# Kernel tuning notes

Hardware: AMD Instinct MI355X
Metric: run time of the kernel (lower is better)

Reference implementation:

```python
import jax, jax.numpy as jnp
import numpy as np

B, T, D_IN, D_OUT = 32, 1024, 512, 512


def _glorot(key, shape):
    fan_in, fan_out = shape[0], shape[1]
    limit = np.sqrt(6.0 / (fan_in + fan_out)).astype(np.float32)
    return jax.random.uniform(key, shape, jnp.float32, -limit, limit)


def setup_inputs() -> dict:
    key = jax.random.key(0)
    ks = jax.random.split(key, 10)
    inp = {
        "inputs": jax.random.normal(ks[0], (B, T, D_IN), jnp.float32),
        "init_states": jnp.zeros((2, B, D_OUT), jnp.float32),
        "Wi": _glorot(ks[1], (D_IN, D_OUT)), "Ui": _glorot(ks[2], (D_OUT, D_OUT)), "bi": jnp.ones((D_OUT,), jnp.float32),
        "Wf": _glorot(ks[3], (D_IN, D_OUT)), "Uf": _glorot(ks[4], (D_OUT, D_OUT)), "bf": jnp.ones((D_OUT,), jnp.float32),
        "Wc": _glorot(ks[5], (D_IN, D_OUT)), "Uc": _glorot(ks[6], (D_OUT, D_OUT)), "bc": jnp.ones((D_OUT,), jnp.float32),
        "Wo": _glorot(ks[7], (D_IN, D_OUT)), "Uo": _glorot(ks[8], (D_OUT, D_OUT)), "bo": jnp.ones((D_OUT,), jnp.float32),
    }
    return inp


def reference(inputs, init_states, Wi, Ui, bi, Wf, Uf, bf, Wc, Uc, bc, Wo, Uo, bo):
    # inputs: [B, T, D_in] (time_major=False), init_states: [2, B, H]
    x_t = jnp.transpose(inputs, (1, 0, 2))  # [T, B, D_in]
    h0, c0 = init_states[0], init_states[1]

    def step(carry, x):
        h, c = carry
        i = jax.nn.sigmoid(x @ Wi + h @ Ui + bi)
        f = jax.nn.sigmoid(x @ Wf + h @ Uf + bf)
        g = jnp.tanh(x @ Wc + h @ Uc + bc)
        c_new = f * c + i * g
        o = jax.nn.sigmoid(x @ Wo + h @ Uo + bo)
        h_new = o * jnp.tanh(c_new)
        return (h_new, c_new), h_new

    _, hs = jax.lax.scan(step, (h0, c0), x_t)  # hs: [T, B, H]
    # original: transpose scan output [T,2,B,H] -> [2,B,T,H] then take [0] (hidden stream)
    return jnp.transpose(hs, (1, 0, 2))  # [B, T, H]
```

## Files before the change

### kernel.cpp

```cpp
#include <hip/hip_runtime.h>


#define T_STEPS 1024
#define BATCH   32
#define DIN     512
#define H       512
#define NWG     64
#define HC      8
#define XSTRIDE 520
#define GSTRIDE 34
#define RECS_PER_PARITY 8192

typedef _Float16 half8  __attribute__((ext_vector_type(8)));
typedef _Float16 half4v __attribute__((ext_vector_type(4)));
typedef float    f32x4  __attribute__((ext_vector_type(4)));
typedef unsigned int u32;
typedef unsigned long long u64;
typedef u32 u32x4 __attribute__((ext_vector_type(4)));

#define AT_LD_U64(p)   __hip_atomic_load((const u64*)(p), __ATOMIC_RELAXED, __HIP_MEMORY_SCOPE_AGENT)
#define AT_ST_U64(p,v) __hip_atomic_store((u64*)(p), (v), __ATOMIC_RELAXED, __HIP_MEMORY_SCOPE_AGENT)

__device__ __forceinline__ float sigmoidf_(float x) {
    return 1.0f / (1.0f + __expf(-x));
}
__device__ __forceinline__ float tanhf_(float x) {
    return 1.0f - 2.0f / (1.0f + __expf(2.0f * x));
}

__global__ __launch_bounds__(512, 1) void lstm_pregate(
    const float* __restrict__ x,
    const float* __restrict__ Wi, const float* __restrict__ Wf,
    const float* __restrict__ Wc, const float* __restrict__ Wo,
    const float* __restrict__ bi, const float* __restrict__ bf,
    const float* __restrict__ bc, const float* __restrict__ bo,
    float* __restrict__ preg, int t0, int tc)
{
    __shared__ _Float16 xbuf[2 * BATCH * XSTRIDE];

    const int tid  = threadIdx.x;
    const int wg   = blockIdx.x;
    const int cb   = wg & 31;
    const int tq   = wg >> 5;
    const int tcq  = tc >> 3;
    const int tb   = t0 + tq * tcq;
    const int lane = tid & 63;
    const int wave = tid >> 6;
    const int mt   = wave & 1;
    const int gsel = wave >> 1;
    const int n_local = lane & 15;
    const int kq   = lane >> 4;
    const int row  = mt * 16 + n_local;
    const int hcol = cb * 16 + n_local;

    const float* Wmat = (gsel == 0) ? Wi : (gsel == 1) ? Wf : (gsel == 2) ? Wc : Wo;
    const float* bvec = (gsel == 0) ? bi : (gsel == 1) ? bf : (gsel == 2) ? bc : bo;
    const float bv = bvec[hcol];

    half8 bfrag[16];
    #pragma unroll
    for (int kk = 0; kk < 16; ++kk) {
        #pragma unroll
        for (int jj = 0; jj < 8; ++jj) {
            int k = kk * 32 + kq * 8 + jj;
            bfrag[kk][jj] = (_Float16)Wmat[k * H + hcol];
        }
    }

    auto stage = [&](int t, int buf) {
        const int sb = tid >> 4;
        const int so = (tid & 15) * 4;
        const float* xr = x + ((size_t)sb * T_STEPS + t) * DIN;
        _Float16* xb = &xbuf[buf * (BATCH * XSTRIDE)];
        #pragma unroll
        for (int q = 0; q < 8; ++q) {
            int colq = so + q * 64;
            float4 v = *(const float4*)(xr + colq);
            half4v hv = { (_Float16)v.x, (_Float16)v.y,
                          (_Float16)v.z, (_Float16)v.w };
            *(half4v*)&xb[sb * XSTRIDE + colq] = hv;
        }
    };

    stage(tb, 0);
    stage(tb + 1, 1);
    __syncthreads();

    for (int lt = 0; lt < tcq; ++lt) {
        f32x4 a0 = {0.f, 0.f, 0.f, 0.f};
        f32x4 a1 = {0.f, 0.f, 0.f, 0.f};
        const _Float16* xr2 =
            &xbuf[(lt & 1) * (BATCH * XSTRIDE) + row * XSTRIDE + kq * 8];
        #pragma unroll
        for (int kk = 0; kk < 16; kk += 2) {
            half8 v0 = *(const half8*)(xr2 + kk * 32);
            half8 v1 = *(const half8*)(xr2 + (kk + 1) * 32);
            a0 = __builtin_amdgcn_mfma_f32_16x16x32_f16(v0, bfrag[kk],     a0, 0, 0, 0);
            a1 = __builtin_amdgcn_mfma_f32_16x16x32_f16(v1, bfrag[kk + 1], a1, 0, 0, 0);
        }
        f32x4 aw;
        #pragma unroll
        for (int r = 0; r < 4; ++r) aw[r] = a0[r] + a1[r] + bv;

        const size_t base =
            (((size_t)(tb - t0 + lt) * 4 + gsel) * 512 + hcol) * 32
            + mt * 16 + kq * 4;
        *(f32x4*)&preg[base] = aw;

        __syncthreads();
        if (lt + 2 < tcq) stage(tb + lt + 2, lt & 1);
    }
}

__global__ __launch_bounds__(256, 1) void lstm_recur(
    const float* __restrict__ init_states,
    const float* __restrict__ Ui, const float* __restrict__ Uf,
    const float* __restrict__ Uc, const float* __restrict__ Uo,
    const float* __restrict__ preg,
    float* __restrict__ out,
    u64* __restrict__ hrec,
    float* __restrict__ cst,
    int t0, int tc)
{
    __shared__ u32 share[2][2][16][64][4];

    const int tid  = threadIdx.x;
    const int wg   = blockIdx.x;
    const int lane = tid & 63;
    const int wave = tid >> 6;
    const int mt   = wave & 1;
    const int nt   = wave >> 1;
    const int n_local = lane & 15;
    const int kq   = lane >> 4;
    const int row  = mt * 16 + n_local;

    const int gi   = n_local >> 2;
    const int cl   = n_local & 3;
    const int ejl  = nt * 4 + cl;
    const int wcol = wg * HC + ejl;
    const int eb   = mt * 16 + kq * 4 + gi;
    const int ecol = wcol;

    float c_state = (t0 == 0) ? init_states[BATCH * H + eb * H + ecol]
                              : cst[eb * H + ecol];

    const int widx = (wg >> 2) * 512 + (ejl >> 1) * 128 + eb * 4 + (wg & 3);

    if (t0 == 0) {
        _Float16 h0 = (_Float16)init_states[eb * H + ecol];
        u32 hu  = (u32)__builtin_bit_cast(unsigned short, h0);
        u32 oth = __shfl_down(hu, 1);
        if ((lane & 1) == 0)
            AT_ST_U64(&hrec[widx], ((u64)1u << 32) | (u64)(hu | (oth << 16)));
    }

    const float* Umat = (gi == 0) ? Ui : (gi == 1) ? Uf : (gi == 2) ? Uc : Uo;
    half8 bfrag[16];
    #pragma unroll
    for (int kk = 0; kk < 16; ++kk) {
        #pragma unroll
        for (int jj = 0; jj < 8; ++jj) {
            int k = kk * 32 + kq * 8 + jj;
            bfrag[kk][jj] = (_Float16)Umat[k * H + wcol];
        }
    }

    const size_t pgbase =
        ((size_t)gi * 512 + wcol) * 32 + mt * 16 + kq * 4;
    f32x4 pg = *(const f32x4*)&preg[pgbase];

    const int ridx_base = row * 4 + kq;
    const int kk0 = nt * 8;
    const bool q0 = (lane >> 2) & 1;
    const bool q1 = (lane >> 3) & 1;

    for (int lt = 0; lt < tc; ++lt) {
        const int gt = t0 + lt;
        const u64* rb = hrec + (size_t)(gt & 1) * RECS_PER_PARITY;
        const u32 target = (u32)(gt + 1);
        const int par = gt & 1;

        u64 rec[32];
        unsigned spins = 0;
        for (;;) {
            #pragma unroll
            for (int kk2 = 0; kk2 < 8; ++kk2) {
                #pragma unroll
                for (int s = 0; s < 4; ++s)
                    rec[kk2 * 4 + s] =
                        AT_LD_U64(&rb[(kk0 + kk2) * 512 + s * 128 + ridx_base]);
            }
            int ok = 1;
            #pragma unroll
            for (int i = 0; i < 32; ++i)
                ok &= ((u32)(rec[i] >> 32) == target);
            if (__all(ok)) break;
            if (++spins > 300000u) break;
        }

        #pragma unroll
        for (int kk2 = 0; kk2 < 8; ++kk2) {
            u32x4 v = { (u32)rec[kk2 * 4 + 0], (u32)rec[kk2 * 4 + 1],
                        (u32)rec[kk2 * 4 + 2], (u32)rec[kk2 * 4 + 3] };
            *(u32x4*)&share[par][mt][kk0 + kk2][lane][0] = v;
        }

        f32x4 pgn = pg;
        if (lt + 1 < tc)
            pgn = *(const f32x4*)&preg[(size_t)(lt + 1) * 65536 + pgbase];

        __syncthreads();

        u32x4 au[16];
        #pragma unroll
        for (int kk = 0; kk < 16; ++kk)
            au[kk] = *(const u32x4*)&share[par][mt][kk][lane][0];

        f32x4 acc  = pg;
        f32x4 acc2 = {0.f, 0.f, 0.f, 0.f};
        #pragma unroll
        for (int kk = 0; kk < 16; kk += 2) {
            union { u32x4 v; half8 h; } a0, a1;
            a0.v = au[kk];
            a1.v = au[kk + 1];
            acc  = __builtin_amdgcn_mfma_f32_16x16x32_f16(a0.h, bfrag[kk],     acc,  0, 0, 0);
            acc2 = __builtin_amdgcn_mfma_f32_16x16x32_f16(a1.h, bfrag[kk + 1], acc2, 0, 0, 0);
        }
        float a0v = acc[0] + acc2[0];
        float a1v = acc[1] + acc2[1];
        float a2v = acc[2] + acc2[2];
        float a3v = acc[3] + acc2[3];

        float t0_ = __shfl_xor(a1v, 4);
        float t1_ = __shfl_xor(a0v, 4);
        float t2_ = __shfl_xor(a3v, 4);
        float t3_ = __shfl_xor(a2v, 4);
        float b0 = q0 ? t0_ : a0v;
        float b1 = q0 ? a1v : t1_;
        float b2 = q0 ? t2_ : a2v;
        float b3 = q0 ? a3v : t3_;
        float u0 = __shfl_xor(b2, 8);
        float u1 = __shfl_xor(b3, 8);
        float u2 = __shfl_xor(b0, 8);
        float u3 = __shfl_xor(b1, 8);
        float pi  = q1 ? u0 : b0;
        float pf  = q1 ? u1 : b1;
        float pgg = q1 ? b2 : u2;
        float po  = q1 ? b3 : u3;

        float ig = sigmoidf_(pi);
        float fg = sigmoidf_(pf);
        float gg = tanhf_(pgg);
        float og = sigmoidf_(po);
        c_state  = fg * c_state + ig * gg;
        float h_val = og * tanhf_(c_state);

        if (gt + 1 < T_STEPS) {
            _Float16 hh = (_Float16)h_val;
            u32 hu  = (u32)__builtin_bit_cast(unsigned short, hh);
            u32 oth = __shfl_down(hu, 1);
            if ((lane & 1) == 0) {
                AT_ST_U64(&hrec[(size_t)((gt + 1) & 1) * RECS_PER_PARITY + widx],
                          ((u64)(u32)(gt + 2) << 32) | (u64)(hu | (oth << 16)));
            }
        }

        out[((size_t)eb * T_STEPS + gt) * H + ecol] = h_val;
        pg = pgn;
    }

    cst[eb * H + ecol] = c_state;
}

__global__ __launch_bounds__(256, 1) void lstm_persistent_fb(
    const float* __restrict__ x,
    const float* __restrict__ init_states,
    const float* __restrict__ Wi, const float* __restrict__ Ui, const float* __restrict__ bi,
    const float* __restrict__ Wf, const float* __restrict__ Uf, const float* __restrict__ bf,
    const float* __restrict__ Wc, const float* __restrict__ Uc, const float* __restrict__ bc,
    const float* __restrict__ Wo, const float* __restrict__ Uo, const float* __restrict__ bo,
    float* __restrict__ out,
    u64* __restrict__ hrec)
{
    __shared__ _Float16 xbuf[2 * BATCH * XSTRIDE];
    __shared__ float    gbuf[2 * BATCH * GSTRIDE];

    const int tid  = threadIdx.x;
    const int wg   = blockIdx.x;
    const int lane = tid & 63;
    const int wave = tid >> 6;
    const int mt   = wave & 1;
    const int nt   = wave >> 1;
    const int row  = mt * 16 + (lane & 15);
    const int kq   = lane >> 4;

    const int eb   = tid >> 3;
    const int ej   = tid & 7;
    const int ecol = wg * HC + ej;

    float c_state = init_states[BATCH * H + eb * H + ecol];
    {
        _Float16 h0 = (_Float16)init_states[eb * H + ecol];
        u32 hu  = (u32)__builtin_bit_cast(unsigned short, h0);
        u32 oth = __shfl_down(hu, 1);
        if ((tid & 1) == 0) {
            const int ridx = (wg >> 2) * 512 + (ej >> 1) * 128 + eb * 4 + (wg & 3);
            AT_ST_U64(&hrec[ridx], ((u64)1u << 32) | (u64)(hu | (oth << 16)));
        }
    }

    const int n_local = lane & 15;
    const int gi   = nt * 2 + (n_local >> 3);
    const int wcol = wg * HC + (n_local & 7);
    const float* Wmat = (gi == 0) ? Wi : (gi == 1) ? Wf : (gi == 2) ? Wc : Wo;
    const float* Umat = (gi == 0) ? Ui : (gi == 1) ? Uf : (gi == 2) ? Uc : Uo;

    half8 bfrag[32];
    #pragma unroll
    for (int kk = 0; kk < 16; ++kk) {
        #pragma unroll
        for (int jj = 0; jj < 8; ++jj) {
            int k = kk * 32 + kq * 8 + jj;
            bfrag[kk][jj]      = (_Float16)Wmat[k * H + wcol];
            bfrag[16 + kk][jj] = (_Float16)Umat[k * H + wcol];
        }
    }

    const float bi_v = bi[ecol], bf_v = bf[ecol], bc_v = bc[ecol], bo_v = bo[ecol];

    auto stage = [&](int t, int buf) {
        const int sb = tid >> 3;
        const int so = (tid & 7) * 4;
        const float* xr = x + ((size_t)sb * T_STEPS + t) * DIN;
        _Float16* xb = &xbuf[buf * (BATCH * XSTRIDE)];
        #pragma unroll
        for (int q = 0; q < 16; ++q) {
            int colq = so + q * 32;
            float4 v = *(const float4*)(xr + colq);
            half4v hv = { (_Float16)v.x, (_Float16)v.y,
                          (_Float16)v.z, (_Float16)v.w };
            *(half4v*)&xb[sb * XSTRIDE + colq] = hv;
        }
    };
    auto xmm = [&](int buf) -> f32x4 {
        f32x4 ax  = {0.f, 0.f, 0.f, 0.f};
        f32x4 ax2 = {0.f, 0.f, 0.f, 0.f};
        const _Float16* xr2 = &xbuf[buf * (BATCH * XSTRIDE) + row * XSTRIDE + kq * 8];
        #pragma unroll
        for (int kk = 0; kk < 16; kk += 2) {
            half8 a0 = *(const half8*)(xr2 + kk * 32);
            half8 a1 = *(const half8*)(xr2 + (kk + 1) * 32);
            ax  = __builtin_amdgcn_mfma_f32_16x16x32_f16(a0, bfrag[kk],     ax,  0, 0, 0);
            ax2 = __builtin_amdgcn_mfma_f32_16x16x32_f16(a1, bfrag[kk + 1], ax2, 0, 0, 0);
        }
        #pragma unroll
        for (int r = 0; r < 4; ++r) ax[r] += ax2[r];
        return ax;
    };

    stage(0, 0);
    stage(1, 1);
    __syncthreads();
    f32x4 acc_x = xmm(0);

    const int ridx_base = row * 4 + kq;
    const int widx = (wg >> 2) * 512 + (ej >> 1) * 128 + eb * 4 + (wg & 3);

    for (int t = 0; t < T_STEPS; ++t) {
        const u64* rb = hrec + (size_t)(t & 1) * RECS_PER_PARITY;
        const u32 target = (u32)(t + 1);

        u64 rec[64];
        unsigned spins = 0;
        for (;;) {
            #pragma unroll
            for (int kk = 0; kk < 16; ++kk) {
                #pragma unroll
                for (int s = 0; s < 4; ++s)
                    rec[kk * 4 + s] = AT_LD_U64(&rb[kk * 512 + s * 128 + ridx_base]);
            }
            int ok = 1;
            #pragma unroll
            for (int i = 0; i < 64; ++i)
                ok &= ((u32)(rec[i] >> 32) == target);
            if (__all(ok)) break;
            if (++spins > 300000u) break;
        }

        float* gb = &gbuf[(t & 1) * (BATCH * GSTRIDE)];
        {
            f32x4 acc  = acc_x;
            f32x4 acc2 = {0.f, 0.f, 0.f, 0.f};
            #pragma unroll
            for (int kk = 0; kk < 16; kk += 2) {
                union { u32 d[4]; half8 h; } a0, a1;
                #pragma unroll
                for (int s = 0; s < 4; ++s) {
                    a0.d[s] = (u32)rec[kk * 4 + s];
                    a1.d[s] = (u32)rec[(kk + 1) * 4 + s];
                }
                acc  = __builtin_amdgcn_mfma_f32_16x16x32_f16(a0.h, bfrag[16 + kk],     acc,  0, 0, 0);
                acc2 = __builtin_amdgcn_mfma_f32_16x16x32_f16(a1.h, bfrag[16 + kk + 1], acc2, 0, 0, 0);
            }
            #pragma unroll
            for (int r = 0; r < 4; ++r) {
                gb[(mt * 16 + kq * 4 + r) * GSTRIDE + nt * 16 + n_local] =
                    acc[r] + acc2[r];
            }
        }
        __syncthreads();

        float h_val;
        {
            float pi = gb[eb * GSTRIDE + ej]      + bi_v;
            float pf = gb[eb * GSTRIDE + 8 + ej]  + bf_v;
            float pg = gb[eb * GSTRIDE + 16 + ej] + bc_v;
            float po = gb[eb * GSTRIDE + 24 + ej] + bo_v;
            float ig = sigmoidf_(pi);
            float fg = sigmoidf_(pf);
            float gg = tanhf_(pg);
            float og = sigmoidf_(po);
            c_state  = fg * c_state + ig * gg;
            h_val    = og * tanhf_(c_state);

            if (t + 1 < T_STEPS) {
                _Float16 hh = (_Float16)h_val;
                u32 hu  = (u32)__builtin_bit_cast(unsigned short, hh);
                u32 oth = __shfl_down(hu, 1);
                if ((tid & 1) == 0) {
                    AT_ST_U64(&hrec[(size_t)((t + 1) & 1) * RECS_PER_PARITY + widx],
                              ((u64)(u32)(t + 2) << 32) | (u64)(hu | (oth << 16)));
                }
            }
        }

        out[((size_t)eb * T_STEPS + t) * H + ecol] = h_val;
        if (t + 1 < T_STEPS) {
            acc_x = xmm((t + 1) & 1);
            if (t + 2 < T_STEPS) stage(t + 2, t & 1);
        }
    }
}

extern "C" void kernel_launch(void* const* d_in, const int* in_sizes, int n_in,
                              void* d_out, int out_size, void* d_ws, size_t ws_size,
                              hipStream_t stream) {
    const float* x           = (const float*)d_in[0];
    const float* init_states = (const float*)d_in[1];
    const float* Wi = (const float*)d_in[2];
    const float* Ui = (const float*)d_in[3];
    const float* bi = (const float*)d_in[4];
    const float* Wf = (const float*)d_in[5];
    const float* Uf = (const float*)d_in[6];
    const float* bf = (const float*)d_in[7];
    const float* Wc = (const float*)d_in[8];
    const float* Uc = (const float*)d_in[9];
    const float* bc = (const float*)d_in[10];
    const float* Wo = (const float*)d_in[11];
    const float* Uo = (const float*)d_in[12];
    const float* bo = (const float*)d_in[13];
    float* out = (float*)d_out;

    const size_t HREC_BYTES = (size_t)2 * RECS_PER_PARITY * 8;
    const size_t CST_BYTES  = (size_t)BATCH * H * 4;

    static const int cands[] = {1024, 512, 256, 128, 64, 32, 16};
    int tc = 0;
    size_t preg_bytes = 0;
    for (int i = 0; i < 7; ++i) {
        size_t pb = (size_t)cands[i] * 2048 * 32 * 4;
        if (ws_size >= pb + HREC_BYTES + CST_BYTES) { tc = cands[i]; preg_bytes = pb; break; }
    }

    if (tc > 0) {
        float* preg = (float*)d_ws;
        u64*   hrec = (u64*)((char*)d_ws + preg_bytes);
        float* cst  = (float*)((char*)d_ws + preg_bytes + HREC_BYTES);

        const int nchunks = T_STEPS / tc;
        for (int c = 0; c < nchunks; ++c) {
            lstm_pregate<<<dim3(256), dim3(512), 0, stream>>>(
                x, Wi, Wf, Wc, Wo, bi, bf, bc, bo, preg, c * tc, tc);
            lstm_recur<<<dim3(NWG), dim3(256), 0, stream>>>(
                init_states, Ui, Uf, Uc, Uo, preg, out, hrec, cst, c * tc, tc);
        }
    } else {
        u64* hrec = (u64*)d_ws;
        lstm_persistent_fb<<<dim3(NWG), dim3(256), 0, stream>>>(
            x, init_states, Wi, Ui, bi, Wf, Uf, bf, Wc, Uc, bc, Wo, Uo, bo,
            out, hrec);
    }
}
```

Before: 2.990 ms.

## Fuse pregate and recurrence into one persistent kernel with ring-buffer producer/consumer

Replaces the two-kernel-per-chunk scheme with a single persistent launch. 64 workgroups run the recurrence while 192 producer workgroups compute the input projections into a 512-slot ring buffer, signalling readiness with per-timestep flags and throttling on a progress counter. The aim is to overlap the input GEMM with the serial recurrence and remove the launch and chunk barriers between them. It adds spin-waits on global flags with timeout escapes, and relies on all 256 workgroups being co-resident; if they are not, it could deadlock or hit the timeouts and produce wrong results.

```diff
diff --git a/kernel.cpp b/kernel.cpp
--- a/kernel.cpp
+++ b/kernel.cpp
@@ -6,10 +6,12 @@
 #define DIN     512
 #define H       512
 #define NWG     64
+#define NPRE    192
 #define HC      8
 #define XSTRIDE 520
 #define GSTRIDE 34
 #define RECS_PER_PARITY 8192
+#define RING_SLOTS 512
 
 typedef _Float16 half8  __attribute__((ext_vector_type(8)));
 typedef _Float16 half4v __attribute__((ext_vector_type(4)));
@@ -26,6 +28,304 @@
 }
 __device__ __forceinline__ float tanhf_(float x) {
     return 1.0f - 2.0f / (1.0f + __expf(2.0f * x));
+}
+
+__global__ __launch_bounds__(256, 1) void lstm_fused(
+    const float* __restrict__ x,
+    const float* __restrict__ init_states,
+    const float* __restrict__ Wi, const float* __restrict__ Wf,
+    const float* __restrict__ Wc, const float* __restrict__ Wo,
+    const float* __restrict__ Ui, const float* __restrict__ Uf,
+    const float* __restrict__ Uc, const float* __restrict__ Uo,
+    const float* __restrict__ bi, const float* __restrict__ bf,
+    const float* __restrict__ bc, const float* __restrict__ bo,
+    float* __restrict__ out,
+    float* __restrict__ preg,
+    u64*   __restrict__ hrec,
+    u32*   __restrict__ pflag,
+    int*   __restrict__ progress)
+{
+    __shared__ __align__(16) char smem[2 * BATCH * XSTRIDE * 2];
+
+    const int tid  = threadIdx.x;
+    const int wg   = blockIdx.x;
+    const int lane = tid & 63;
+    const int wave = tid >> 6;
+
+    if (wg < NWG) {
+        u32* share = (u32*)smem;
+        auto shp = [&](int par, int mtv, int kk, int ln) -> u32* {
+            return &share[(((par * 2 + mtv) * 16 + kk) * 64 + ln) * 4];
+        };
+
+        const int mt = wave & 1;
+        const int nt = wave >> 1;
+        const int n_local = lane & 15;
+        const int kq = lane >> 4;
+        const int row = mt * 16 + n_local;
+
+        const int gi   = n_local >> 2;
+        const int cl   = n_local & 3;
+        const int ejl  = nt * 4 + cl;
+        const int wcol = wg * HC + ejl;
+        const int eb   = mt * 16 + kq * 4 + gi;
+        const int ecol = wcol;
+
+        float c_state = init_states[BATCH * H + eb * H + ecol];
+        const int widx = (wg >> 2) * 512 + (ejl >> 1) * 128 + eb * 4 + (wg & 3);
+
+        {
+            _Float16 h0 = (_Float16)init_states[eb * H + ecol];
+            u32 hu  = (u32)__builtin_bit_cast(unsigned short, h0);
+            u32 oth = __shfl_down(hu, 1);
+            if ((lane & 1) == 0)
+                AT_ST_U64(&hrec[widx], ((u64)1u << 32) | (u64)(hu | (oth << 16)));
+        }
+
+        const float* Umat = (gi == 0) ? Ui : (gi == 1) ? Uf : (gi == 2) ? Uc : Uo;
+        half8 bfrag[16];
+        #pragma unroll
+        for (int kk = 0; kk < 16; ++kk) {
+            #pragma unroll
+            for (int jj = 0; jj < 8; ++jj) {
+                int k = kk * 32 + kq * 8 + jj;
+                bfrag[kk][jj] = (_Float16)Umat[k * H + wcol];
+            }
+        }
+
+        const size_t pgbase =
+            ((size_t)gi * 512 + wcol) * 32 + mt * 16 + kq * 4;
+        const u64* pregq = (const u64*)preg;
+
+        auto waitpreg = [&](int t) {
+            const u32 tgt = (u32)(t + 1);
+            const u32* fp = pflag + (size_t)t * 32;
+            unsigned sp = 0;
+            for (;;) {
+                u32 v = (lane < 32)
+                    ? __hip_atomic_load(&fp[lane], __ATOMIC_RELAXED,
+                                        __HIP_MEMORY_SCOPE_AGENT)
+                    : tgt;
+                if (__all(v == tgt)) break;
+                if (++sp > 2000000u) break;
+            }
+        };
+        auto ldpg = [&](int t) -> f32x4 {
+            size_t qi = (((size_t)(t & (RING_SLOTS - 1))) * 65536 + pgbase) >> 1;
+            union { u64 q[2]; f32x4 v; } u;
+            u.q[0] = AT_LD_U64(&pregq[qi]);
+            u.q[1] = AT_LD_U64(&pregq[qi + 1]);
+            return u.v;
+        };
+
+        waitpreg(0);
+        f32x4 pg = ldpg(0);
+
+        const int ridx_base = row * 4 + kq;
+        const int kk0 = nt * 8;
+        const bool q0 = (lane >> 2) & 1;
+        const bool q1 = (lane >> 3) & 1;
+
+        for (int t = 0; t < T_STEPS; ++t) {
+            const u64* rb = hrec + (size_t)(t & 1) * RECS_PER_PARITY;
+            const u32 target = (u32)(t + 1);
+            const int par = t & 1;
+
+            u64 rec[32];
+            unsigned spins = 0;
+            for (;;) {
+                #pragma unroll
+                for (int kk2 = 0; kk2 < 8; ++kk2) {
+                    #pragma unroll
+                    for (int s = 0; s < 4; ++s)
+                        rec[kk2 * 4 + s] =
+                            AT_LD_U64(&rb[(kk0 + kk2) * 512 + s * 128 + ridx_base]);
+                }
+                int ok = 1;
+                #pragma unroll
+                for (int i = 0; i < 32; ++i)
+                    ok &= ((u32)(rec[i] >> 32) == target);
+                if (__all(ok)) break;
+                if (++spins > 300000u) break;
+            }
+
+            #pragma unroll
+            for (int kk2 = 0; kk2 < 8; ++kk2) {
+                u32x4 v = { (u32)rec[kk2 * 4 + 0], (u32)rec[kk2 * 4 + 1],
+                            (u32)rec[kk2 * 4 + 2], (u32)rec[kk2 * 4 + 3] };
+                *(u32x4*)shp(par, mt, kk0 + kk2, lane) = v;
+            }
+
+            f32x4 pgn = pg;
+            if (t + 1 < T_STEPS) {
+                waitpreg(t + 1);
+                pgn = ldpg(t + 1);
+            }
+
+            __syncthreads();
+
+            u32x4 au[16];
+            #pragma unroll
+            for (int kk = 0; kk < 16; ++kk)
+                au[kk] = *(const u32x4*)shp(par, mt, kk, lane);
+
+            f32x4 acc  = pg;
+            f32x4 acc2 = {0.f, 0.f, 0.f, 0.f};
+            #pragma unroll
+            for (int kk = 0; kk < 16; kk += 2) {
+                union { u32x4 v; half8 h; } a0, a1;
+                a0.v = au[kk];
+                a1.v = au[kk + 1];
+                acc  = __builtin_amdgcn_mfma_f32_16x16x32_f16(a0.h, bfrag[kk],     acc,  0, 0, 0);
+                acc2 = __builtin_amdgcn_mfma_f32_16x16x32_f16(a1.h, bfrag[kk + 1], acc2, 0, 0, 0);
+            }
+            float a0v = acc[0] + acc2[0];
+            float a1v = acc[1] + acc2[1];
+            float a2v = acc[2] + acc2[2];
+            float a3v = acc[3] + acc2[3];
+
+            float t0_ = __shfl_xor(a1v, 4);
+            float t1_ = __shfl_xor(a0v, 4);
+            float t2_ = __shfl_xor(a3v, 4);
+            float t3_ = __shfl_xor(a2v, 4);
+            float b0 = q0 ? t0_ : a0v;
+            float b1 = q0 ? a1v : t1_;
+            float b2 = q0 ? t2_ : a2v;
+            float b3 = q0 ? a3v : t3_;
+            float u0 = __shfl_xor(b2, 8);
+            float u1 = __shfl_xor(b3, 8);
+            float u2 = __shfl_xor(b0, 8);
+            float u3 = __shfl_xor(b1, 8);
+            float pi  = q1 ? u0 : b0;
+            float pf  = q1 ? u1 : b1;
+            float pgg = q1 ? b2 : u2;
+            float po  = q1 ? b3 : u3;
+
+            float ig = sigmoidf_(pi);
+            float fg = sigmoidf_(pf);
+            float gg = tanhf_(pgg);
+            float og = sigmoidf_(po);
+            c_state  = fg * c_state + ig * gg;
+            float h_val = og * tanhf_(c_state);
+
+            if (t + 1 < T_STEPS) {
+                _Float16 hh = (_Float16)h_val;
+                u32 hu  = (u32)__builtin_bit_cast(unsigned short, hh);
+                u32 oth = __shfl_down(hu, 1);
+                if ((lane & 1) == 0) {
+                    AT_ST_U64(&hrec[(size_t)((t + 1) & 1) * RECS_PER_PARITY + widx],
+                              ((u64)(u32)(t + 2) << 32) | (u64)(hu | (oth << 16)));
+                }
+            }
+
+            out[((size_t)eb * T_STEPS + t) * H + ecol] = h_val;
+            if (wg == 0 && tid == 0)
+                __hip_atomic_store(progress, t, __ATOMIC_RELAXED,
+                                   __HIP_MEMORY_SCOPE_AGENT);
+            pg = pgn;
+        }
+    } else {
+        _Float16* xbuf = (_Float16*)smem;
+
+        const int g2  = wg - NWG;
+        const int cb  = g2 & 31;
+        const int tsl = g2 >> 5;
+        const int mt  = wave & 1;
+        const int gp  = wave >> 1;
+        const int n_local = lane & 15;
+        const int kq  = lane >> 4;
+        const int row = mt * 16 + n_local;
+        const int hcol = cb * 16 + n_local;
+
+        const float* W0  = (gp == 0) ? Wi : Wc;
+        const float* W1  = (gp == 0) ? Wf : Wo;
+        const float* b0p = (gp == 0) ? bi : bc;
+        const float* b1p = (gp == 0) ? bf : bo;
+        const float bv0 = b0p[hcol];
+        const float bv1 = b1p[hcol];
+
+        half8 bw0[16], bw1[16];
+        #pragma unroll
+        for (int kk = 0; kk < 16; ++kk) {
+            #pragma unroll
+            for (int jj = 0; jj < 8; ++jj) {
+                int k = kk * 32 + kq * 8 + jj;
+                bw0[kk][jj] = (_Float16)W0[k * H + hcol];
+                bw1[kk][jj] = (_Float16)W1[k * H + hcol];
+            }
+        }
+
+        auto stage = [&](int t, int buf) {
+            const int sb = tid >> 3;
+            const int so = (tid & 7) * 4;
+            const float* xr = x + ((size_t)sb * T_STEPS + t) * DIN;
+            _Float16* xb = &xbuf[buf * (BATCH * XSTRIDE)];
+            #pragma unroll
+            for (int q = 0; q < 16; ++q) {
+                int colq = so + q * 32;
+                float4 v = *(const float4*)(xr + colq);
+                half4v hv = { (_Float16)v.x, (_Float16)v.y,
+                              (_Float16)v.z, (_Float16)v.w };
+                *(half4v*)&xb[sb * XSTRIDE + colq] = hv;
+            }
+        };
+
+        stage(tsl, 0);
+        stage(tsl + 6, 1);
+        __syncthreads();
+
+        u64* pregq = (u64*)preg;
+
+        for (int k = 0, t = tsl; t < T_STEPS; ++k, t += 6) {
+            if (t > 510) {
+                unsigned sp = 0;
+                for (;;) {
+                    int p = __hip_atomic_load(progress, __ATOMIC_RELAXED,
+                                              __HIP_MEMORY_SCOPE_AGENT);
+                    if (p < 0 || p >= T_STEPS) p = 0;
+                    if (t <= p + 510) break;
+                    if (++sp > 4000000u) break;
+                    __builtin_amdgcn_s_sleep(8);
+                }
+            }
+
+            const _Float16* xr2 =
+                &xbuf[(k & 1) * (BATCH * XSTRIDE) + row * XSTRIDE + kq * 8];
+            f32x4 a0 = {0.f,0.f,0.f,0.f}, a1 = {0.f,0.f,0.f,0.f};
+            f32x4 a2 = {0.f,0.f,0.f,0.f}, a3 = {0.f,0.f,0.f,0.f};
+            #pragma unroll
+            for (int kk = 0; kk < 16; kk += 2) {
+                half8 v0 = *(const half8*)(xr2 + kk * 32);
+                half8 v1 = *(const half8*)(xr2 + (kk + 1) * 32);
+                a0 = __builtin_amdgcn_mfma_f32_16x16x32_f16(v0, bw0[kk],     a0, 0, 0, 0);
+                a1 = __builtin_amdgcn_mfma_f32_16x16x32_f16(v0, bw1[kk],     a1, 0, 0, 0);
+                a2 = __builtin_amdgcn_mfma_f32_16x16x32_f16(v1, bw0[kk + 1], a2, 0, 0, 0);
+                a3 = __builtin_amdgcn_mfma_f32_16x16x32_f16(v1, bw1[kk + 1], a3, 0, 0, 0);
+            }
+
+            const int slot = t & (RING_SLOTS - 1);
+            {
+                union { f32x4 v; u64 q[2]; } u;
+                #pragma unroll
+                for (int r = 0; r < 4; ++r) u.v[r] = a0[r] + a2[r] + bv0;
+                size_t base = (((size_t)slot * 4 + gp * 2) * 512 + hcol) * 32
+                              + mt * 16 + kq * 4;
+                AT_ST_U64(&pregq[base >> 1], u.q[0]);
+                AT_ST_U64(&pregq[(base >> 1) + 1], u.q[1]);
+                #pragma unroll
+                for (int r = 0; r < 4; ++r) u.v[r] = a1[r] + a3[r] + bv1;
+                base += (size_t)512 * 32;
+                AT_ST_U64(&pregq[base >> 1], u.q[0]);
+                AT_ST_U64(&pregq[(base >> 1) + 1], u.q[1]);
+            }
+
+            __syncthreads();
+            if (tid == 0)
+                __hip_atomic_store(&pflag[(size_t)t * 32 + cb], (u32)(t + 1),
+                                   __ATOMIC_RELEASE, __HIP_MEMORY_SCOPE_AGENT);
+            if (t + 12 < T_STEPS) stage(t + 12, k & 1);
+        }
+    }
 }
 
 __global__ __launch_bounds__(512, 1) void lstm_pregate(
@@ -87,8 +387,8 @@
     __syncthreads();
 
     for (int lt = 0; lt < tcq; ++lt) {
-        f32x4 a0 = {0.f, 0.f, 0.f, 0.f};
-        f32x4 a1 = {0.f, 0.f, 0.f, 0.f};
+        f32x4 a0 = {0.f,0.f,0.f,0.f};
+        f32x4 a1 = {0.f,0.f,0.f,0.f};
         const _Float16* xr2 =
             &xbuf[(lt & 1) * (BATCH * XSTRIDE) + row * XSTRIDE + kq * 8];
         #pragma unroll
@@ -461,13 +761,28 @@
     const float* bo = (const float*)d_in[13];
     float* out = (float*)d_out;
 
-    const size_t HREC_BYTES = (size_t)2 * RECS_PER_PARITY * 8;
-    const size_t CST_BYTES  = (size_t)BATCH * H * 4;
-
-    static const int cands[] = {1024, 512, 256, 128, 64, 32, 16};
+    const size_t RING_BYTES  = (size_t)RING_SLOTS * 65536 * 4;
+    const size_t HREC_BYTES  = (size_t)2 * RECS_PER_PARITY * 8;
+    const size_t PFLAG_BYTES = (size_t)T_STEPS * 32 * 4;
+    const size_t PROG_BYTES  = 64;
+    const size_t CST_BYTES   = (size_t)BATCH * H * 4;
+
+    if (ws_size >= RING_BYTES + HREC_BYTES + PFLAG_BYTES + PROG_BYTES) {
+        float* preg = (float*)d_ws;
+        u64*   hrec = (u64*)((char*)d_ws + RING_BYTES);
+        u32*   pflag = (u32*)((char*)d_ws + RING_BYTES + HREC_BYTES);
+        int*   progress = (int*)((char*)d_ws + RING_BYTES + HREC_BYTES + PFLAG_BYTES);
+
+        lstm_fused<<<dim3(NWG + NPRE), dim3(256), 0, stream>>>(
+            x, init_states, Wi, Wf, Wc, Wo, Ui, Uf, Uc, Uo,
+            bi, bf, bc, bo, out, preg, hrec, pflag, progress);
+        return;
+    }
+
+    static const int cands[] = {512, 256, 128, 64, 32, 16};
     int tc = 0;
     size_t preg_bytes = 0;
-    for (int i = 0; i < 7; ++i) {
+    for (int i = 0; i < 6; ++i) {
         size_t pb = (size_t)cands[i] * 2048 * 32 * 4;
         if (ws_size >= pb + HREC_BYTES + CST_BYTES) { tc = cands[i]; preg_bytes = pb; break; }
     }
```

New measurement: 4.038 ms. 35.0% more time.
